# Optimization experiments

Hardware: AMD Instinct MI355X
Metric: run time of the kernel (lower is better)

The kernel has to match this reference:

```python
import jax, jax.numpy as jnp
import numpy as np

K = 8        # k nearest neighbors (module init arg)
HEADS = 8


def setup_inputs() -> dict:
    key = jax.random.key(0)
    ks = jax.random.split(key, 5)
    B, N, D = 2, 4096, 512
    x = jax.random.normal(ks[0], (B, N, D), dtype=jnp.float32)
    coords = jax.random.uniform(ks[1], (B, N, 2), dtype=jnp.float32) * 100.0
    w_qkv = jax.random.normal(ks[2], (3 * D, D), dtype=jnp.float32) * 0.02
    w_proj = jax.random.normal(ks[3], (D, D), dtype=jnp.float32) * 0.02
    b_proj = jax.random.normal(ks[4], (D,), dtype=jnp.float32) * 0.02
    return {"x": x, "coords": coords, "w_qkv": w_qkv, "w_proj": w_proj, "b_proj": b_proj}


def reference(x, coords, w_qkv, w_proj, b_proj):
    B, N, D = x.shape
    H = HEADS
    hd = D // H
    k_actual = min(K + 1, N)

    # pairwise euclidean distances (B, N, N), as torch.cdist
    d2 = (jnp.sum(coords**2, -1)[:, :, None]
          + jnp.sum(coords**2, -1)[:, None, :]
          - 2.0 * jnp.einsum('bnc,bmc->bnm', coords, coords))
    dist = jnp.sqrt(jnp.maximum(d2, 0.0))

    # k-NN indices: topk of -dist  -> (B, N, k_actual)
    _, nn_idx = jax.lax.top_k(-dist, k_actual)

    # gather neighbor features: (B, N, k, D)
    x_nb = jax.vmap(lambda xb, ib: xb[ib])(x, nn_idx)

    # qkv projections (Linear, no bias): y = x @ W^T
    qkv_c = jnp.einsum('bnd,ed->bne', x, w_qkv)          # (B, N, 3D)
    q = qkv_c[..., :D].reshape(B, N, H, hd)              # (B, N, H, hd)
    qkv_n = jnp.einsum('bnkd,ed->bnke', x_nb, w_qkv)     # (B, N, k, 3D)
    k_n = qkv_n[..., D:2 * D].reshape(B, N, k_actual, H, hd)
    v_n = qkv_n[..., 2 * D:].reshape(B, N, k_actual, H, hd)

    # attention over k neighbors
    attn = jnp.einsum('bnhd,bnkhd->bnhk', q, k_n) / jnp.sqrt(jnp.float32(hd))
    attn = jax.nn.softmax(attn, axis=-1)
    out = jnp.einsum('bnhk,bnkhd->bnhd', attn, v_n).reshape(B, N, D)

    # proj(GELU(out)) with exact (erf) GELU as nn.GELU default
    out = jax.nn.gelu(out, approximate=False)
    out = jnp.einsum('bnd,ed->bne', out, w_proj) + b_proj
    return x + out
```

## Files before the change

### kernel.cpp

```cpp
#include <hip/hip_runtime.h>
#include <hip/hip_bf16.h>

using bf16 = __hip_bfloat16;

typedef __attribute__((ext_vector_type(8))) __bf16 bf16x8;
typedef __attribute__((ext_vector_type(4))) float f32x4;

#define NPTS 4096
#define DMODEL 512
#define HDIM 64
#define KNN 9
#define MROWS 8192

#define GRIDW 32
#define CELLW 3.125f
#define NCELL (GRIDW * GRIDW)

#define NN_BYTES    (MROWS * 16 * 4)
#define QKV_BYTES   ((size_t)MROWS * 1536 * 2)
#define G_BYTES     ((size_t)MROWS * 512 * 2)
#define XB_BYTES    ((size_t)MROWS * 512 * 2)
#define WQ_BYTES    ((size_t)1536 * 512 * 2)
#define WP_BYTES    ((size_t)512 * 512 * 2)
#define GSTART_BYTES (2 * 1025 * 4)
#define SXY_BYTES    ((size_t)2 * NPTS * 8)
#define SIDX_BYTES   ((size_t)2 * NPTS * 4)

__global__ __launch_bounds__(1024) void prep_kernel(
    const float4* __restrict__ s0, ushort4* __restrict__ d0, int n0,
    const float4* __restrict__ s1, ushort4* __restrict__ d1, int n1,
    const float4* __restrict__ s2, ushort4* __restrict__ d2, int n2,
    const float* __restrict__ coords,
    int* __restrict__ gstart,
    float2* __restrict__ sxy,
    int* __restrict__ sidx) {
    __shared__ int cnt[NCELL];
    __shared__ int off2[NCELL];
    __shared__ int sstart[NCELL];
    __shared__ int wsum[16];

    if (blockIdx.x < 1280) {
        int g = blockIdx.x * 1024 + threadIdx.x;
        const float4* s; ushort4* d; int i;
        if (g < n0) { s = s0; d = d0; i = g; }
        else if (g < n0 + n1) { s = s1; d = d1; i = g - n0; }
        else { s = s2; d = d2; i = g - n0 - n1; }
        float4 v = s[i];
        bf16 b0 = __float2bfloat16(v.x), b1 = __float2bfloat16(v.y);
        bf16 b2 = __float2bfloat16(v.z), b3 = __float2bfloat16(v.w);
        ushort4 o;
        o.x = *reinterpret_cast<unsigned short*>(&b0);
        o.y = *reinterpret_cast<unsigned short*>(&b1);
        o.z = *reinterpret_cast<unsigned short*>(&b2);
        o.w = *reinterpret_cast<unsigned short*>(&b3);
        d[i] = o;
        return;
    }

    const int b = blockIdx.x - 1280, tid = threadIdx.x;
    cnt[tid] = 0; off2[tid] = 0;
    __syncthreads();
    const float2* c2 = (const float2*)(coords + (size_t)b * NPTS * 2);
    float px[4], py[4]; int pc[4];
#pragma unroll
    for (int i = 0; i < 4; ++i) {
        int p = tid + i * 1024;
        float2 v = c2[p];
        px[i] = v.x; py[i] = v.y;
        int cx = min(GRIDW - 1, (int)(v.x / CELLW));
        int cy = min(GRIDW - 1, (int)(v.y / CELLW));
        pc[i] = cy * GRIDW + cx;
        atomicAdd(&cnt[pc[i]], 1);
    }
    __syncthreads();
    const int v = cnt[tid];
    const int lane = tid & 63, wv = tid >> 6;
    int inc = v;
#pragma unroll
    for (int o = 1; o < 64; o <<= 1) {
        int t = __shfl_up(inc, o, 64);
        if (lane >= o) inc += t;
    }
    if (lane == 63) wsum[wv] = inc;
    __syncthreads();
    if (tid < 16) {
        int w = wsum[tid];
#pragma unroll
        for (int o = 1; o < 16; o <<= 1) {
            int t = __shfl_up(w, o, 16);
            if (tid >= o) w += t;
        }
        wsum[tid] = w;
    }
    __syncthreads();
    const int excl = inc - v + (wv ? wsum[wv - 1] : 0);
    sstart[tid] = excl;
    gstart[b * 1025 + tid] = excl;
    if (tid == 1023) gstart[b * 1025 + 1024] = excl + v;
    __syncthreads();
#pragma unroll
    for (int i = 0; i < 4; ++i) {
        int o = atomicAdd(&off2[pc[i]], 1);
        int pos = sstart[pc[i]] + o;
        sxy[(size_t)b * NPTS + pos]  = make_float2(px[i], py[i]);
        sidx[(size_t)b * NPTS + pos] = tid + i * 1024;
    }
}

__global__ __launch_bounds__(256) void knn_grid(const float* __restrict__ coords,
                                                const int* __restrict__ gstart,
                                                const float2* __restrict__ sxy,
                                                const int* __restrict__ sidx,
                                                int* __restrict__ nn_out) {
    const int wv = threadIdx.x >> 6, lane = threadIdx.x & 63;
    const int q = blockIdx.x * 4 + wv;
    const int b = q >> 12, n = q & 4095;
    const float2* cb = (const float2*)(coords + (size_t)b * NPTS * 2);
    const float2 pq = cb[n];
    const float xn = pq.x, yn = pq.y;
    const float sn = __fadd_rn(__fmul_rn(xn, xn), __fmul_rn(yn, yn));
    const int cx = min(GRIDW - 1, (int)(xn / CELLW));
    const int cy = min(GRIDW - 1, (int)(yn / CELLW));
    const int* gs = gstart + b * 1025;
    const float2* xy = sxy + (size_t)b * NPTS;
    const int* id = sidx + (size_t)b * NPTS;

    float d9 = 0.0f;
    int outi[9];
    for (int r = 2;; ++r) {
        float bd[10]; int bi[10];
#pragma unroll
        for (int j = 0; j < 10; ++j) { bd[j] = 3.4e38f; bi[j] = 0x7fffffff; }
        const int ylo = max(cy - r, 0), yhi = min(cy + r, GRIDW - 1);
        const int xlo = max(cx - r, 0), xhi = min(cx + r, GRIDW - 1);
        for (int ry = ylo; ry <= yhi; ++ry) {
            const int s0 = gs[ry * GRIDW + xlo];
            const int s1 = gs[ry * GRIDW + xhi + 1];
            for (int p0 = s0; p0 < s1; p0 += 64) {
                const int pp = p0 + lane;
                float d = 3.4e38f; int idx = 0x7fffffff;
                if (pp < s1) {
                    float2 cm = xy[pp];
                    idx = id[pp];
                    float sc  = __fadd_rn(__fmul_rn(cm.x, cm.x), __fmul_rn(cm.y, cm.y));
                    float dot = __fadd_rn(__fmul_rn(xn, cm.x), __fmul_rn(yn, cm.y));
                    float d2  = __fsub_rn(__fadd_rn(sn, sc), __fmul_rn(2.0f, dot));
                    d = sqrtf(fmaxf(d2, 0.0f));
                }
                if (d < bd[8]) {
#pragma unroll
                    for (int j = 8; j >= 1; --j) {
                        if (d < bd[j]) {
                            bool t2 = d < bd[j - 1];
                            bd[j] = t2 ? bd[j - 1] : d;
                            bi[j] = t2 ? bi[j - 1] : idx;
                        }
                    }
                    if (d < bd[0]) { bd[0] = d; bi[0] = idx; }
                }
            }
        }
        unsigned long long head =
            ((unsigned long long)__float_as_uint(bd[0]) << 32) | (unsigned)bi[0];
#pragma unroll
        for (int rr = 0; rr < 9; ++rr) {
            unsigned long long m = head;
#pragma unroll
            for (int s2 = 32; s2 > 0; s2 >>= 1) {
                unsigned long long o = __shfl_xor(m, s2, 64);
                m = o < m ? o : m;
            }
            outi[rr] = (int)(unsigned)(m & 0xffffffffULL);
            if (rr == 8) d9 = __uint_as_float((unsigned)(m >> 32));
            if (m == head) {
#pragma unroll
                for (int j = 0; j < 9; ++j) { bd[j] = bd[j + 1]; bi[j] = bi[j + 1]; }
                head = ((unsigned long long)__float_as_uint(bd[0]) << 32) | (unsigned)bi[0];
            }
        }
        if (d9 <= (float)r * CELLW - 0.01f || r >= 34) break;
    }
    if (lane == 0) {
        int* o = nn_out + (size_t)q * 16;
#pragma unroll
        for (int rr = 0; rr < 9; ++rr) o[rr] = outi[rr];
    }
}

__device__ __forceinline__ void gload16(const bf16* g, bf16* l) {
    __builtin_amdgcn_global_load_lds(
        (const __attribute__((address_space(1))) unsigned int*)g,
        (__attribute__((address_space(3))) unsigned int*)l,
        16, 0, 0);
}

template <bool EPI, int NCOLT>
__global__ __launch_bounds__(256) void gemm_bt(const bf16* __restrict__ A,
                                               const bf16* __restrict__ W,
                                               void* __restrict__ Cout,
                                               int Nn, int Kd,
                                               const float* __restrict__ bias,
                                               const float* __restrict__ resid) {
    __shared__ __attribute__((aligned(16))) bf16 As[2][128][32];
    __shared__ __attribute__((aligned(16))) bf16 Bs[2][128][32];

    const int tid = threadIdx.x;
    const int bid = blockIdx.x;
    const int xcd = bid & 7;
    const int idx = bid >> 3;
    const int rowBase = (xcd * 8 + (idx & 7)) * 128;
    const int colBase = (idx >> 3) * 128;
    const int nk = Kd >> 5;

    const int lane = tid & 63, w = tid >> 6;
    const int wr = w >> 1, wc = w & 1;

    const int r0  = tid >> 2;
    const int kk0 = (tid & 3) * 8;

    f32x4 acc[4][4] = {};

    const bf16* gaBase = A + (size_t)(rowBase + r0) * Kd + kk0;
    const bf16* gbBase = W + (size_t)(colBase + r0) * Kd + kk0;

#define STAGE(bufi, kt)                                                     \
    do {                                                                    \
        const bf16* ga = gaBase + (size_t)(kt) * 32;                        \
        const bf16* gb = gbBase + (size_t)(kt) * 32;                        \
        gload16(ga,                   &As[bufi][r0][kk0]);                  \
        gload16(ga + (size_t)64 * Kd, &As[bufi][r0 + 64][kk0]);             \
        gload16(gb,                   &Bs[bufi][r0][kk0]);                  \
        gload16(gb + (size_t)64 * Kd, &Bs[bufi][r0 + 64][kk0]);             \
    } while (0)

    STAGE(0, 0);
    __syncthreads();

    int buf = 0;
    const int r16 = lane & 15;
    const int hk  = (lane >> 4) * 8;
    for (int kt = 0; kt < nk; ++kt) {
        if (kt + 1 < nk) STAGE(buf ^ 1, kt + 1);

        bf16x8 afr[4], bfr[4];
#pragma unroll
        for (int m2 = 0; m2 < 4; ++m2)
            afr[m2] = *(const bf16x8*)&As[buf][wr * 64 + m2 * 16 + r16][hk];
#pragma unroll
        for (int n2 = 0; n2 < 4; ++n2)
            bfr[n2] = *(const bf16x8*)&Bs[buf][wc * 64 + n2 * 16 + r16][hk];
#pragma unroll
        for (int m2 = 0; m2 < 4; ++m2)
#pragma unroll
            for (int n2 = 0; n2 < 4; ++n2)
                acc[m2][n2] = __builtin_amdgcn_mfma_f32_16x16x32_bf16(
                    afr[m2], bfr[n2], acc[m2][n2], 0, 0, 0);

        __syncthreads();
        buf ^= 1;
    }
#undef STAGE

    const int r4  = (lane >> 4) * 4;
    const int c16 = lane & 15;
#pragma unroll
    for (int m2 = 0; m2 < 4; ++m2) {
#pragma unroll
        for (int n2 = 0; n2 < 4; ++n2) {
            const int gc = colBase + wc * 64 + n2 * 16 + c16;
#pragma unroll
            for (int r = 0; r < 4; ++r) {
                const int gr = rowBase + wr * 64 + m2 * 16 + r4 + r;
                float v = acc[m2][n2][r];
                if (EPI) {
                    v = v + bias[gc];
                    v = resid[(size_t)gr * Nn + gc] + v;
                    ((float*)Cout)[(size_t)gr * Nn + gc] = v;
                } else {
                    ((bf16*)Cout)[(size_t)gr * Nn + gc] = __float2bfloat16(v);
                }
            }
        }
    }
}

__global__ __launch_bounds__(256) void attn_kernel(const bf16* __restrict__ qkv,
                                                   const int* __restrict__ nn,
                                                   const int* __restrict__ sidx,
                                                   bf16* __restrict__ g) {
    const int wv = threadIdx.x >> 6, lane = threadIdx.x & 63;
    const int pos = blockIdx.x * 4 + wv;
    const int b = pos >> 12;
    const int q = b * NPTS + sidx[(size_t)b * NPTS + (pos & 4095)];
    const int rowbase = b * NPTS;

    const int* nnq = nn + (size_t)q * 16;
    int idxs[KNN];
#pragma unroll
    for (int j = 0; j < KNN; ++j) idxs[j] = nnq[j];

    bf16x8 qv = *(const bf16x8*)(qkv + (size_t)q * 1536 + lane * 8);
    float qf[8];
#pragma unroll
    for (int e = 0; e < 8; ++e) qf[e] = (float)qv[e];

    float lg[KNN];
#pragma unroll
    for (int j = 0; j < KNN; ++j) {
        const bf16x8 kv = *(const bf16x8*)(
            qkv + (size_t)(rowbase + idxs[j]) * 1536 + DMODEL + lane * 8);
        float p = 0.0f;
#pragma unroll
        for (int e = 0; e < 8; ++e) p += qf[e] * (float)kv[e];
        p += __shfl_xor(p, 1, 64);
        p += __shfl_xor(p, 2, 64);
        p += __shfl_xor(p, 4, 64);
        lg[j] = p * 0.125f;
    }
    float mx = lg[0];
#pragma unroll
    for (int j = 1; j < KNN; ++j) mx = fmaxf(mx, lg[j]);
    float wgt[KNN], ssum = 0.0f;
#pragma unroll
    for (int j = 0; j < KNN; ++j) { wgt[j] = expf(lg[j] - mx); ssum += wgt[j]; }
    const float inv = 1.0f / ssum;

    float o[8] = {};
#pragma unroll
    for (int j = 0; j < KNN; ++j) {
        const bf16x8 vv = *(const bf16x8*)(
            qkv + (size_t)(rowbase + idxs[j]) * 1536 + 2 * DMODEL + lane * 8);
        const float wj = wgt[j] * inv;
#pragma unroll
        for (int e = 0; e < 8; ++e) o[e] += wj * (float)vv[e];
    }
    bf16x8 ov;
#pragma unroll
    for (int e = 0; e < 8; ++e) {
        float ge = 0.5f * o[e] * (1.0f + erff(o[e] * 0.70710678118654752f));
        ov[e] = (__bf16)__float2bfloat16(ge);
    }
    *(bf16x8*)(g + (size_t)q * DMODEL + lane * 8) = ov;
}

extern "C" void kernel_launch(void* const* d_in, const int* in_sizes, int n_in,
                              void* d_out, int out_size, void* d_ws, size_t ws_size,
                              hipStream_t stream) {
    const float* x      = (const float*)d_in[0];
    const float* coords = (const float*)d_in[1];
    const float* w_qkv  = (const float*)d_in[2];
    const float* w_proj = (const float*)d_in[3];
    const float* b_proj = (const float*)d_in[4];
    float* out = (float*)d_out;

    char* wsb = (char*)d_ws;
    size_t off = 0;
    int*    nn     = (int*)(wsb + off);    off += NN_BYTES;
    bf16*   qkv    = (bf16*)(wsb + off);   off += QKV_BYTES;
    bf16*   g      = (bf16*)(wsb + off);   off += G_BYTES;
    bf16*   xb     = (bf16*)(wsb + off);   off += XB_BYTES;
    bf16*   wqb    = (bf16*)(wsb + off);   off += WQ_BYTES;
    bf16*   wpb    = (bf16*)(wsb + off);   off += WP_BYTES;
    int*    gstart = (int*)(wsb + off);    off += GSTART_BYTES;
    float2* sxy    = (float2*)(wsb + off); off += SXY_BYTES;
    int*    sidx   = (int*)(wsb + off);    off += SIDX_BYTES;

    const int n0 = 4194304 / 4, n1 = 786432 / 4, n2 = 262144 / 4;
    prep_kernel<<<1282, 1024, 0, stream>>>(
        (const float4*)x, (ushort4*)xb, n0,
        (const float4*)w_qkv, (ushort4*)wqb, n1,
        (const float4*)w_proj, (ushort4*)wpb, n2,
        coords, gstart, sxy, sidx);

    knn_grid<<<2048, 256, 0, stream>>>(coords, gstart, sxy, sidx, nn);
    gemm_bt<false, 12><<<768, 256, 0, stream>>>(xb, wqb, qkv, 1536, 512,
                                                nullptr, nullptr);
    attn_kernel<<<2048, 256, 0, stream>>>(qkv, nn, sidx, g);
    gemm_bt<true, 4><<<256, 256, 0, stream>>>(g, wpb, out, 512, 512,
                                              b_proj, x);
}
```

Before: 150.7 us.

## Work in grid-sorted point order so kNN and attention gathers are spatially local

The kNN kernel now processes points in cell-sorted order and stores neighbor indices as sorted positions rather than original ids. The QKV GEMM gathers its A rows through the sort permutation, so the qkv buffer is laid out in sorted order. The attention kernel reads queries and neighbors contiguously in that order and scatters its output back to original rows. This removes the sidx indirection in the kNN inner loop and makes neighbor K/V gathers hit nearby rows for better cache locality, at the cost of a permuted row load in the GEMM. Tie-breaking among equal distances now compares sorted positions instead of original indices, which could change which neighbor is chosen when distances are equal.

```diff
diff --git a/kernel.cpp b/kernel.cpp
--- a/kernel.cpp
+++ b/kernel.cpp
@@ -107,23 +107,19 @@
     }
 }
 
-__global__ __launch_bounds__(256) void knn_grid(const float* __restrict__ coords,
-                                                const int* __restrict__ gstart,
+__global__ __launch_bounds__(256) void knn_grid(const int* __restrict__ gstart,
                                                 const float2* __restrict__ sxy,
-                                                const int* __restrict__ sidx,
                                                 int* __restrict__ nn_out) {
     const int wv = threadIdx.x >> 6, lane = threadIdx.x & 63;
-    const int q = blockIdx.x * 4 + wv;
-    const int b = q >> 12, n = q & 4095;
-    const float2* cb = (const float2*)(coords + (size_t)b * NPTS * 2);
-    const float2 pq = cb[n];
+    const int pos = blockIdx.x * 4 + wv;
+    const int b = pos >> 12, p = pos & 4095;
+    const float2* xy = sxy + (size_t)b * NPTS;
+    const float2 pq = xy[p];
     const float xn = pq.x, yn = pq.y;
     const float sn = __fadd_rn(__fmul_rn(xn, xn), __fmul_rn(yn, yn));
     const int cx = min(GRIDW - 1, (int)(xn / CELLW));
     const int cy = min(GRIDW - 1, (int)(yn / CELLW));
     const int* gs = gstart + b * 1025;
-    const float2* xy = sxy + (size_t)b * NPTS;
-    const int* id = sidx + (size_t)b * NPTS;
 
     float d9 = 0.0f;
     int outi[9];
@@ -141,7 +137,7 @@
                 float d = 3.4e38f; int idx = 0x7fffffff;
                 if (pp < s1) {
                     float2 cm = xy[pp];
-                    idx = id[pp];
+                    idx = pp;
                     float sc  = __fadd_rn(__fmul_rn(cm.x, cm.x), __fmul_rn(cm.y, cm.y));
                     float dot = __fadd_rn(__fmul_rn(xn, cm.x), __fmul_rn(yn, cm.y));
                     float d2  = __fsub_rn(__fadd_rn(sn, sc), __fmul_rn(2.0f, dot));
@@ -181,7 +177,7 @@
         if (d9 <= (float)r * CELLW - 0.01f || r >= 34) break;
     }
     if (lane == 0) {
-        int* o = nn_out + (size_t)q * 16;
+        int* o = nn_out + (size_t)pos * 16;
 #pragma unroll
         for (int rr = 0; rr < 9; ++rr) o[rr] = outi[rr];
     }
@@ -194,13 +190,14 @@
         16, 0, 0);
 }
 
-template <bool EPI, int NCOLT>
+template <bool EPI, bool PERM>
 __global__ __launch_bounds__(256) void gemm_bt(const bf16* __restrict__ A,
                                                const bf16* __restrict__ W,
                                                void* __restrict__ Cout,
                                                int Nn, int Kd,
                                                const float* __restrict__ bias,
-                                               const float* __restrict__ resid) {
+                                               const float* __restrict__ resid,
+                                               const int* __restrict__ perm) {
     __shared__ __attribute__((aligned(16))) bf16 As[2][128][32];
     __shared__ __attribute__((aligned(16))) bf16 Bs[2][128][32];
 
@@ -220,15 +217,19 @@
 
     f32x4 acc[4][4] = {};
 
-    const bf16* gaBase = A + (size_t)(rowBase + r0) * Kd + kk0;
-    const bf16* gbBase = W + (size_t)(colBase + r0) * Kd + kk0;
+    const int row0 = rowBase + r0, row1 = rowBase + r0 + 64;
+    const int pr0 = PERM ? ((row0 & ~4095) + perm[row0]) : row0;
+    const int pr1 = PERM ? ((row1 & ~4095) + perm[row1]) : row1;
+
+    const bf16* gaBase0 = A + (size_t)pr0 * Kd + kk0;
+    const bf16* gaBase1 = A + (size_t)pr1 * Kd + kk0;
+    const bf16* gbBase  = W + (size_t)(colBase + r0) * Kd + kk0;
 
 #define STAGE(bufi, kt)                                                     \
     do {                                                                    \
-        const bf16* ga = gaBase + (size_t)(kt) * 32;                        \
+        gload16(gaBase0 + (size_t)(kt) * 32, &As[bufi][r0][kk0]);           \
+        gload16(gaBase1 + (size_t)(kt) * 32, &As[bufi][r0 + 64][kk0]);      \
         const bf16* gb = gbBase + (size_t)(kt) * 32;                        \
-        gload16(ga,                   &As[bufi][r0][kk0]);                  \
-        gload16(ga + (size_t)64 * Kd, &As[bufi][r0 + 64][kk0]);             \
         gload16(gb,                   &Bs[bufi][r0][kk0]);                  \
         gload16(gb + (size_t)64 * Kd, &Bs[bufi][r0 + 64][kk0]);             \
     } while (0)
@@ -291,15 +292,14 @@
     const int wv = threadIdx.x >> 6, lane = threadIdx.x & 63;
     const int pos = blockIdx.x * 4 + wv;
     const int b = pos >> 12;
-    const int q = b * NPTS + sidx[(size_t)b * NPTS + (pos & 4095)];
     const int rowbase = b * NPTS;
 
-    const int* nnq = nn + (size_t)q * 16;
+    const int* nnq = nn + (size_t)pos * 16;
     int idxs[KNN];
 #pragma unroll
     for (int j = 0; j < KNN; ++j) idxs[j] = nnq[j];
 
-    bf16x8 qv = *(const bf16x8*)(qkv + (size_t)q * 1536 + lane * 8);
+    bf16x8 qv = *(const bf16x8*)(qkv + (size_t)pos * 1536 + lane * 8);
     float qf[8];
 #pragma unroll
     for (int e = 0; e < 8; ++e) qf[e] = (float)qv[e];
@@ -340,7 +340,8 @@
         float ge = 0.5f * o[e] * (1.0f + erff(o[e] * 0.70710678118654752f));
         ov[e] = (__bf16)__float2bfloat16(ge);
     }
-    *(bf16x8*)(g + (size_t)q * DMODEL + lane * 8) = ov;
+    const int orig = sidx[pos];
+    *(bf16x8*)(g + (size_t)(rowbase + orig) * DMODEL + lane * 8) = ov;
 }
 
 extern "C" void kernel_launch(void* const* d_in, const int* in_sizes, int n_in,
@@ -372,10 +373,10 @@
         (const float4*)w_proj, (ushort4*)wpb, n2,
         coords, gstart, sxy, sidx);
 
-    knn_grid<<<2048, 256, 0, stream>>>(coords, gstart, sxy, sidx, nn);
-    gemm_bt<false, 12><<<768, 256, 0, stream>>>(xb, wqb, qkv, 1536, 512,
-                                                nullptr, nullptr);
+    knn_grid<<<2048, 256, 0, stream>>>(gstart, sxy, nn);
+    gemm_bt<false, true><<<768, 256, 0, stream>>>(xb, wqb, qkv, 1536, 512,
+                                                  nullptr, nullptr, sidx);
     attn_kernel<<<2048, 256, 0, stream>>>(qkv, nn, sidx, g);
-    gemm_bt<true, 4><<<256, 256, 0, stream>>>(g, wpb, out, 512, 512,
-                                              b_proj, x);
-}
+    gemm_bt<true, false><<<256, 256, 0, stream>>>(g, wpb, out, 512, 512,
+                                                  b_proj, x, nullptr);
+}
```

Measured after the change: 149.2 us. Within noise of the previous version (-1.0%).
